# Kernel optimization log

Measured on AMD Instinct MI355X. Metric: run time of the kernel, lower is better.

Reference implementation:

```python
import jax, jax.numpy as jnp
import numpy as np
from jax import lax

N, H, W, C = 4, 256, 256, 128
COUT = 128
BS_IN, BS_OUT, BSTR = 18, 16, 16  # gather block, conv-out block, block stride
N_ACTIVE = 512


def setup_inputs() -> dict:
    key = jax.random.key(0)
    ks = jax.random.split(key, 8)
    x = jax.random.normal(ks[0], (N, H, W, C), dtype=jnp.float32)
    w = jax.random.normal(ks[1], (3, 3, C, COUT), dtype=jnp.float32) * 0.05  # HWIO
    b = jax.random.normal(ks[2], (COUT,), dtype=jnp.float32) * 0.05
    gamma = jax.random.uniform(ks[3], (COUT,), dtype=jnp.float32, minval=0.5, maxval=1.5)
    beta = jax.random.normal(ks[4], (COUT,), dtype=jnp.float32) * 0.1
    mean = jax.random.normal(ks[5], (COUT,), dtype=jnp.float32) * 0.1
    var = jax.random.uniform(ks[6], (COUT,), dtype=jnp.float32, minval=0.5, maxval=1.5)
    # unique active block ids over the N x (H/16) x (W/16) grid -> disjoint scatter targets
    n_blocks = N * (H // BSTR) * (W // BSTR)
    active = jax.random.permutation(ks[7], n_blocks)[:N_ACTIVE].astype(jnp.int32)
    return {"x": x, "w": w, "b": b, "gamma": gamma, "beta": beta,
            "mean": mean, "var": var, "active": active}


def reference(x, w, b, gamma, beta, mean, var, active):
    n_, h_, w_, c_ = x.shape
    nby, nbx = h_ // BSTR, w_ // BSTR
    bn = active // (nby * nbx)
    rem = active % (nby * nbx)
    by = rem // nbx
    bx = rem % nbx

    # --- sparse_gather: overlapping BS_IN x BS_IN input blocks (zero-pad edges) ---
    pad = BS_IN - BS_OUT
    xp = jnp.pad(x, ((0, 0), (0, pad), (0, pad), (0, 0)))
    Hp, Wp = h_ + pad, w_ + pad
    d_in = jnp.arange(BS_IN, dtype=jnp.int32)
    hs = by[:, None] * BSTR + d_in[None, :]            # [Nb, 18]
    ws = bx[:, None] * BSTR + d_in[None, :]            # [Nb, 18]
    gidx = bn[:, None, None] * (Hp * Wp) + hs[:, :, None] * Wp + ws[:, None, :]
    p = xp.reshape(-1, c_)[gidx]                       # [Nb, 18, 18, C]

    # --- dense conv + BN(eval, eps=1e-3) + ReLU on gathered blocks ---
    q = lax.conv_general_dilated(p, w, window_strides=(1, 1), padding='VALID',
                                 dimension_numbers=('NHWC', 'HWIO', 'NHWC'))
    q = q + b
    q = (q - mean) * (gamma * lax.rsqrt(var + 1e-3)) + beta
    q = jax.nn.relu(q)                                 # [Nb, 16, 16, COUT]

    # --- sparse_scatter: write disjoint BS_OUT blocks back into a copy of x ---
    d_out = jnp.arange(BS_OUT, dtype=jnp.int32)
    hso = by[:, None] * BSTR + d_out[None, :]
    wso = bx[:, None] * BSTR + d_out[None, :]
    sidx = bn[:, None, None] * (h_ * w_) + hso[:, :, None] * w_ + wso[:, None, :]
    y = x.reshape(-1, c_).at[sidx.reshape(-1)].set(q.reshape(-1, q.shape[-1]))
    return y.reshape(n_, h_, w_, c_)
```

## Files before the change

### kernel.cpp

```cpp
#include <hip/hip_runtime.h>
#include <hip/hip_bf16.h>

#define H_ 256
#define W_ 256
#define C_ 128
#define NBPOS 1024
#define NACT 512

typedef __bf16 bf16x8 __attribute__((ext_vector_type(8)));
typedef float f32x4 __attribute__((ext_vector_type(4)));

#define SCALE_OFF 294912
#define SHIFT_OFF 295424
#define FLAGS_OFF 295936

__global__ void prep_kernel(const float* __restrict__ w, const float* __restrict__ b,
                            const float* __restrict__ gamma, const float* __restrict__ beta,
                            const float* __restrict__ mean, const float* __restrict__ var,
                            const int* __restrict__ active,
                            __bf16* __restrict__ wprep, float* __restrict__ scale,
                            float* __restrict__ shift, int* __restrict__ flags) {
  int blk = blockIdx.x, tid = threadIdx.x;
  if (blk < 576) {
    int o = blk * 256 + tid;
    int j = o & 7, cout = (o >> 3) & 127, k8 = (o >> 10) & 15, tap = o >> 14;
    wprep[o] = (__bf16)w[((size_t)tap * 128 + k8 * 8 + j) * 128 + cout];
  } else {
    if (tid < 128) {
      float s = gamma[tid] * rsqrtf(var[tid] + 1e-3f);
      scale[tid] = s;
      shift[tid] = (b[tid] - mean[tid]) * s + beta[tid];
    }
    for (int i = tid; i < NACT; i += 256) flags[active[i]] = 1;
  }
}

__global__ __launch_bounds__(256, 2) void fused_kernel(
    const float* __restrict__ x, const __bf16* __restrict__ wprep,
    const float* __restrict__ scale, const float* __restrict__ shift,
    const int* __restrict__ flags, float* __restrict__ y) {
  __shared__ unsigned char ldsA[324 * 128];
  __shared__ unsigned char ldsB[2][8192];

  const int pb = blockIdx.x;
  const int tid = threadIdx.x;
  const int bn = pb >> 8, by = (pb >> 4) & 15, bx = pb & 15;
  const int h0 = by * 16, w0 = bx * 16;

  if (!flags[pb]) {
    size_t base4 = ((((size_t)bn * H_ + h0) * W_ + w0) * C_) >> 2;
    const float4* __restrict__ xs = (const float4*)x;
    float4* __restrict__ ys = (float4*)y;
#pragma unroll 8
    for (int i = 0; i < 32; ++i) {
      int lin = (i << 8) + tid;
      int row = lin >> 9, rem = lin & 511;
      size_t idx4 = base4 + (size_t)row * (W_ * C_ / 4) + rem;
      ys[idx4] = xs[idx4];
    }
    return;
  }

  const int lane = tid & 63;
  const int wid = tid >> 6;
  const float* xb = x + (size_t)bn * (H_ * W_ * C_);

  float sc[8], sh[8];
  {
    int col = lane & 15;
#pragma unroll
    for (int nb = 0; nb < 8; ++nb) {
      sc[nb] = scale[nb * 16 + col];
      sh[nb] = shift[nb * 16 + col];
    }
  }

  f32x4 acc[4][8];
  f32x4 zero = {0.f, 0.f, 0.f, 0.f};
#pragma unroll
  for (int i = 0; i < 4; ++i)
#pragma unroll
    for (int j = 0; j < 8; ++j) acc[i][j] = zero;

  const uint4* wp4 = (const uint4*)wprep;
  uint4 t0, t1;
  auto load_t = [&](int u) {
    int ks = u % 18, h = u / 18;
    int tile = ((ks >> 1) << 2) + (h << 1) + (ks & 1);
    t0 = wp4[tile * 512 + tid];
    t1 = wp4[tile * 512 + 256 + tid];
  };
  auto stage = [&](int half) {
    for (int chunk = tid; chunk < 324 * 8; chunk += 256) {
      int s = chunk >> 3, c8 = chunk & 7;
      int iy = s / 18, ix = s - iy * 18;
      int hs = h0 + iy, wsp = w0 + ix;
      float4 f0 = make_float4(0.f, 0.f, 0.f, 0.f), f1 = f0;
      if (hs < H_ && wsp < W_) {
        const float* p = xb + (size_t)(hs * W_ + wsp) * C_ + half * 64 + c8 * 8;
        f0 = *(const float4*)p;
        f1 = *(const float4*)(p + 4);
      }
      bf16x8 v;
      v[0] = (__bf16)f0.x; v[1] = (__bf16)f0.y; v[2] = (__bf16)f0.z; v[3] = (__bf16)f0.w;
      v[4] = (__bf16)f1.x; v[5] = (__bf16)f1.y; v[6] = (__bf16)f1.z; v[7] = (__bf16)f1.w;
      int lin = s * 128 + c8 * 16;
      *(bf16x8*)(&ldsA[lin ^ ((s & 7) << 4)]) = v;
    }
  };

  load_t(0);
  stage(0);
  ((uint4*)ldsB[0])[tid] = t0;
  ((uint4*)ldsB[0])[256 + tid] = t1;
  load_t(1);
  __syncthreads();

  const int koff = (lane >> 4) * 16;
  const int colb = (lane & 15) * 16;
  const int krow = (lane >> 4) * 2048;

  for (int u = 0; u < 36; ++u) {
    int cur = u & 1;
    if (u < 35) {
      ((uint4*)ldsB[cur ^ 1])[tid] = t0;
      ((uint4*)ldsB[cur ^ 1])[256 + tid] = t1;
      if (u < 34) load_t(u + 2);
    }
    int ks = u % 18;
    int tap = ks >> 1, kch = ks & 1;
    int dyv = tap / 3, dxv = tap - dyv * 3;

    bf16x8 a[4];
#pragma unroll
    for (int mi = 0; mi < 4; ++mi) {
      int srow = (wid * 4 + mi + dyv) * 18 + dxv + (lane & 15);
      int lin = srow * 128 + kch * 64 + koff;
      a[mi] = *(const bf16x8*)(&ldsA[lin ^ ((srow & 7) << 4)]);
    }
    bf16x8 bfr[8];
#pragma unroll
    for (int nb = 0; nb < 8; ++nb)
      bfr[nb] = *(const bf16x8*)(&ldsB[cur][krow + nb * 256 + colb]);
#pragma unroll
    for (int mi = 0; mi < 4; ++mi)
#pragma unroll
      for (int nb = 0; nb < 8; ++nb)
        acc[mi][nb] = __builtin_amdgcn_mfma_f32_16x16x32_bf16(a[mi], bfr[nb], acc[mi][nb], 0, 0, 0);

    __syncthreads();
    if (u == 17) {
      stage(1);
      __syncthreads();
    }
  }

  const int colc = lane & 15;
  float* yb = y + (((size_t)bn * H_ + h0) * W_ + w0) * C_;
#pragma unroll
  for (int mi = 0; mi < 4; ++mi) {
    int oy = wid * 4 + mi;
#pragma unroll
    for (int r = 0; r < 4; ++r) {
      int ox = (lane >> 4) * 4 + r;
      float* yr = yb + ((size_t)oy * W_ + ox) * C_;
#pragma unroll
      for (int nb = 0; nb < 8; ++nb) {
        float v = acc[mi][nb][r] * sc[nb] + sh[nb];
        yr[nb * 16 + colc] = fmaxf(v, 0.f);
      }
    }
  }
}

extern "C" void kernel_launch(void* const* d_in, const int* in_sizes, int n_in,
                              void* d_out, int out_size, void* d_ws, size_t ws_size,
                              hipStream_t stream) {
  const float* x     = (const float*)d_in[0];
  const float* w     = (const float*)d_in[1];
  const float* b     = (const float*)d_in[2];
  const float* gamma = (const float*)d_in[3];
  const float* beta  = (const float*)d_in[4];
  const float* mean  = (const float*)d_in[5];
  const float* var   = (const float*)d_in[6];
  const int*   act   = (const int*)d_in[7];
  float* y = (float*)d_out;
  char* ws = (char*)d_ws;
  __bf16* wprep = (__bf16*)ws;
  float* scale = (float*)(ws + SCALE_OFF);
  float* shift = (float*)(ws + SHIFT_OFF);
  int* flags = (int*)(ws + FLAGS_OFF);

  hipMemsetAsync(flags, 0, NBPOS * sizeof(int), stream);
  prep_kernel<<<dim3(577), dim3(256), 0, stream>>>(w, b, gamma, beta, mean, var, act,
                                                   wprep, scale, shift, flags);
  fused_kernel<<<dim3(NBPOS), dim3(256), 0, stream>>>(x, wprep, scale, shift, flags, y);
}
```

Before: 92.14 us.

## Split fused kernel into copy and compact conv kernels, load weights from global

Replaces the single fused kernel with two kernels. A copy kernel handles inactive blocks using nontemporal loads and stores. A conv kernel launches one workgroup per active block, indexed through the active list. The conv kernel drops the double-buffered LDS weight staging and reads weight fragments straight from global memory/L2, and it stages the input halves inside a simple loop. This removes divergent work within one grid and per-step LDS syncs, at the cost of an extra launch, losing overlap between copy and conv, and possibly higher global-load latency for the weights.

Result: no change. 93.68 us (+1.7%).

```diff
diff --git a/kernel.cpp b/kernel.cpp
--- a/kernel.cpp
+++ b/kernel.cpp
@@ -35,34 +35,39 @@
   }
 }
 
-__global__ __launch_bounds__(256, 2) void fused_kernel(
+__global__ __launch_bounds__(256) void copy_kernel(const float* __restrict__ x,
+                                                   const int* __restrict__ flags,
+                                                   float* __restrict__ y) {
+  int pb = blockIdx.x;
+  if (flags[pb]) return;
+  int bn = pb >> 8, by = (pb >> 4) & 15, bx = pb & 15;
+  size_t base4 = ((((size_t)bn * H_ + by * 16) * W_ + bx * 16) * C_) >> 2;
+  const f32x4* __restrict__ xs = (const f32x4*)x;
+  f32x4* __restrict__ ys = (f32x4*)y;
+#pragma unroll 4
+  for (int i = 0; i < 32; ++i) {
+    int lin = (i << 8) + threadIdx.x;
+    int row = lin >> 9, rem = lin & 511;
+    size_t idx4 = base4 + (size_t)row * (W_ * C_ / 4) + rem;
+    f32x4 v = __builtin_nontemporal_load(&xs[idx4]);
+    __builtin_nontemporal_store(v, &ys[idx4]);
+  }
+}
+
+__global__ __launch_bounds__(256, 2) void conv_kernel(
     const float* __restrict__ x, const __bf16* __restrict__ wprep,
     const float* __restrict__ scale, const float* __restrict__ shift,
-    const int* __restrict__ flags, float* __restrict__ y) {
+    const int* __restrict__ active, float* __restrict__ y) {
   __shared__ unsigned char ldsA[324 * 128];
-  __shared__ unsigned char ldsB[2][8192];
 
-  const int pb = blockIdx.x;
   const int tid = threadIdx.x;
-  const int bn = pb >> 8, by = (pb >> 4) & 15, bx = pb & 15;
-  const int h0 = by * 16, w0 = bx * 16;
-
-  if (!flags[pb]) {
-    size_t base4 = ((((size_t)bn * H_ + h0) * W_ + w0) * C_) >> 2;
-    const float4* __restrict__ xs = (const float4*)x;
-    float4* __restrict__ ys = (float4*)y;
-#pragma unroll 8
-    for (int i = 0; i < 32; ++i) {
-      int lin = (i << 8) + tid;
-      int row = lin >> 9, rem = lin & 511;
-      size_t idx4 = base4 + (size_t)row * (W_ * C_ / 4) + rem;
-      ys[idx4] = xs[idx4];
-    }
-    return;
-  }
-
   const int lane = tid & 63;
   const int wid = tid >> 6;
+  const int aid = active[blockIdx.x];
+  const int bn = aid >> 8;
+  const int by = (aid >> 4) & 15;
+  const int bx = aid & 15;
+  const int h0 = by * 16, w0 = bx * 16;
   const float* xb = x + (size_t)bn * (H_ * W_ * C_);
 
   float sc[8], sh[8];
@@ -82,15 +87,12 @@
 #pragma unroll
     for (int j = 0; j < 8; ++j) acc[i][j] = zero;
 
-  const uint4* wp4 = (const uint4*)wprep;
-  uint4 t0, t1;
-  auto load_t = [&](int u) {
-    int ks = u % 18, h = u / 18;
-    int tile = ((ks >> 1) << 2) + (h << 1) + (ks & 1);
-    t0 = wp4[tile * 512 + tid];
-    t1 = wp4[tile * 512 + 256 + tid];
-  };
-  auto stage = [&](int half) {
+  const bf16x8* __restrict__ wq = (const bf16x8*)wprep;
+  const int koff = (lane >> 4) * 16;
+  const int sbl = ((lane >> 4) << 7) + (lane & 15);
+
+  for (int half = 0; half < 2; ++half) {
+    __syncthreads();
     for (int chunk = tid; chunk < 324 * 8; chunk += 256) {
       int s = chunk >> 3, c8 = chunk & 7;
       int iy = s / 18, ix = s - iy * 18;
@@ -107,51 +109,31 @@
       int lin = s * 128 + c8 * 16;
       *(bf16x8*)(&ldsA[lin ^ ((s & 7) << 4)]) = v;
     }
-  };
+    __syncthreads();
 
-  load_t(0);
-  stage(0);
-  ((uint4*)ldsB[0])[tid] = t0;
-  ((uint4*)ldsB[0])[256 + tid] = t1;
-  load_t(1);
-  __syncthreads();
+#pragma unroll 2
+    for (int ks = 0; ks < 18; ++ks) {
+      int tap = ks >> 1, kch = ks & 1;
+      int dyv = tap / 3, dxv = tap - dyv * 3;
+      int tile = tap * 4 + half * 2 + kch;
 
-  const int koff = (lane >> 4) * 16;
-  const int colb = (lane & 15) * 16;
-  const int krow = (lane >> 4) * 2048;
-
-  for (int u = 0; u < 36; ++u) {
-    int cur = u & 1;
-    if (u < 35) {
-      ((uint4*)ldsB[cur ^ 1])[tid] = t0;
-      ((uint4*)ldsB[cur ^ 1])[256 + tid] = t1;
-      if (u < 34) load_t(u + 2);
-    }
-    int ks = u % 18;
-    int tap = ks >> 1, kch = ks & 1;
-    int dyv = tap / 3, dxv = tap - dyv * 3;
-
-    bf16x8 a[4];
+      bf16x8 a[4];
 #pragma unroll
-    for (int mi = 0; mi < 4; ++mi) {
-      int srow = (wid * 4 + mi + dyv) * 18 + dxv + (lane & 15);
-      int lin = srow * 128 + kch * 64 + koff;
-      a[mi] = *(const bf16x8*)(&ldsA[lin ^ ((srow & 7) << 4)]);
-    }
-    bf16x8 bfr[8];
-#pragma unroll
-    for (int nb = 0; nb < 8; ++nb)
-      bfr[nb] = *(const bf16x8*)(&ldsB[cur][krow + nb * 256 + colb]);
-#pragma unroll
-    for (int mi = 0; mi < 4; ++mi)
+      for (int mi = 0; mi < 4; ++mi) {
+        int srow = (wid * 4 + mi + dyv) * 18 + dxv + (lane & 15);
+        int lin = srow * 128 + kch * 64 + koff;
+        a[mi] = *(const bf16x8*)(&ldsA[lin ^ ((srow & 7) << 4)]);
+      }
+      bf16x8 bfr[8];
+      int sb = tile * 512 + sbl;
 #pragma unroll
       for (int nb = 0; nb < 8; ++nb)
-        acc[mi][nb] = __builtin_amdgcn_mfma_f32_16x16x32_bf16(a[mi], bfr[nb], acc[mi][nb], 0, 0, 0);
-
-    __syncthreads();
-    if (u == 17) {
-      stage(1);
-      __syncthreads();
+        bfr[nb] = wq[sb + nb * 16];
+#pragma unroll
+      for (int mi = 0; mi < 4; ++mi)
+#pragma unroll
+        for (int nb = 0; nb < 8; ++nb)
+          acc[mi][nb] = __builtin_amdgcn_mfma_f32_16x16x32_bf16(a[mi], bfr[nb], acc[mi][nb], 0, 0, 0);
     }
   }
 
@@ -167,7 +149,7 @@
 #pragma unroll
       for (int nb = 0; nb < 8; ++nb) {
         float v = acc[mi][nb][r] * sc[nb] + sh[nb];
-        yr[nb * 16 + colc] = fmaxf(v, 0.f);
+        __builtin_nontemporal_store(fmaxf(v, 0.f), &yr[nb * 16 + colc]);
       }
     }
   }
@@ -191,8 +173,9 @@
   float* shift = (float*)(ws + SHIFT_OFF);
   int* flags = (int*)(ws + FLAGS_OFF);
 
-  hipMemsetAsync(flags, 0, NBPOS * sizeof(int), stream);
+  (void)hipMemsetAsync(flags, 0, NBPOS * sizeof(int), stream);
   prep_kernel<<<dim3(577), dim3(256), 0, stream>>>(w, b, gamma, beta, mean, var, act,
                                                    wprep, scale, shift, flags);
-  fused_kernel<<<dim3(NBPOS), dim3(256), 0, stream>>>(x, wprep, scale, shift, flags, y);
+  copy_kernel<<<dim3(NBPOS), dim3(256), 0, stream>>>(x, flags, y);
+  conv_kernel<<<dim3(NACT), dim3(256), 0, stream>>>(x, wprep, scale, shift, act, y);
 }
```

## Pair each active conv block with an inactive copy block, interleaving copies

Applied to the files above, without the earlier changes.

Replaces the flag-based grid of 1024 blocks, where inactive blocks only copied x to y, with 512 blocks that each run one active conv and copy one inactive block. The copy is split into eight chunks whose loads and stores are spread across the MFMA loop, so memory traffic overlaps with compute. Copies and outputs use nontemporal loads and stores. The memset is replaced by a single-block kernel that builds the inactive list from a shared-memory bitmask. This relies on exactly 512 active and 512 inactive blocks, and it adds registers plus one extra launch.

Result: faster. 80.25 us (-12.9%).

```diff
diff --git a/kernel.cpp b/kernel.cpp
--- a/kernel.cpp
+++ b/kernel.cpp
@@ -12,58 +12,75 @@
 
 #define SCALE_OFF 294912
 #define SHIFT_OFF 295424
-#define FLAGS_OFF 295936
-
-__global__ void prep_kernel(const float* __restrict__ w, const float* __restrict__ b,
-                            const float* __restrict__ gamma, const float* __restrict__ beta,
-                            const float* __restrict__ mean, const float* __restrict__ var,
-                            const int* __restrict__ active,
-                            __bf16* __restrict__ wprep, float* __restrict__ scale,
-                            float* __restrict__ shift, int* __restrict__ flags) {
-  int blk = blockIdx.x, tid = threadIdx.x;
-  if (blk < 576) {
-    int o = blk * 256 + tid;
-    int j = o & 7, cout = (o >> 3) & 127, k8 = (o >> 10) & 15, tap = o >> 14;
-    wprep[o] = (__bf16)w[((size_t)tap * 128 + k8 * 8 + j) * 128 + cout];
-  } else {
-    if (tid < 128) {
-      float s = gamma[tid] * rsqrtf(var[tid] + 1e-3f);
-      scale[tid] = s;
-      shift[tid] = (b[tid] - mean[tid]) * s + beta[tid];
-    }
-    for (int i = tid; i < NACT; i += 256) flags[active[i]] = 1;
-  }
-}
-
-__global__ __launch_bounds__(256, 2) void fused_kernel(
+#define INACT_OFF 295936
+
+__global__ void prep_w_kernel(const float* __restrict__ w, __bf16* __restrict__ wprep) {
+  int o = blockIdx.x * 256 + threadIdx.x;
+  int j = o & 7, cout = (o >> 3) & 127, k8 = (o >> 10) & 15, tap = o >> 14;
+  wprep[o] = (__bf16)w[((size_t)tap * 128 + k8 * 8 + j) * 128 + cout];
+}
+
+__global__ void small_kernel(const float* __restrict__ b, const float* __restrict__ gamma,
+                             const float* __restrict__ beta, const float* __restrict__ mean,
+                             const float* __restrict__ var, const int* __restrict__ active,
+                             float* __restrict__ scale, float* __restrict__ shift,
+                             int* __restrict__ inact) {
+  __shared__ unsigned mask[32];
+  __shared__ int cnt;
+  int tid = threadIdx.x;
+  if (tid < 32) mask[tid] = 0u;
+  if (tid == 0) cnt = 0;
+  __syncthreads();
+  if (tid < NACT) {
+    int a = active[tid];
+    atomicOr(&mask[a >> 5], 1u << (a & 31));
+  }
+  if (tid < 128) {
+    float s = gamma[tid] * rsqrtf(var[tid] + 1e-3f);
+    scale[tid] = s;
+    shift[tid] = (b[tid] - mean[tid]) * s + beta[tid];
+  }
+  __syncthreads();
+  if (!((mask[tid >> 5] >> (tid & 31)) & 1u)) {
+    int p = atomicAdd(&cnt, 1);
+    inact[p] = tid;
+  }
+}
+
+__global__ __launch_bounds__(256, 2) void conv_kernel(
     const float* __restrict__ x, const __bf16* __restrict__ wprep,
     const float* __restrict__ scale, const float* __restrict__ shift,
-    const int* __restrict__ flags, float* __restrict__ y) {
+    const int* __restrict__ active, const int* __restrict__ inact,
+    float* __restrict__ y) {
   __shared__ unsigned char ldsA[324 * 128];
   __shared__ unsigned char ldsB[2][8192];
 
-  const int pb = blockIdx.x;
   const int tid = threadIdx.x;
-  const int bn = pb >> 8, by = (pb >> 4) & 15, bx = pb & 15;
-  const int h0 = by * 16, w0 = bx * 16;
-
-  if (!flags[pb]) {
-    size_t base4 = ((((size_t)bn * H_ + h0) * W_ + w0) * C_) >> 2;
-    const float4* __restrict__ xs = (const float4*)x;
-    float4* __restrict__ ys = (float4*)y;
-#pragma unroll 8
-    for (int i = 0; i < 32; ++i) {
-      int lin = (i << 8) + tid;
-      int row = lin >> 9, rem = lin & 511;
-      size_t idx4 = base4 + (size_t)row * (W_ * C_ / 4) + rem;
-      ys[idx4] = xs[idx4];
-    }
-    return;
-  }
-
   const int lane = tid & 63;
   const int wid = tid >> 6;
+  const int aid = active[blockIdx.x];
+  const int bn = aid >> 8, by = (aid >> 4) & 15, bx = aid & 15;
+  const int h0 = by * 16, w0 = bx * 16;
   const float* xb = x + (size_t)bn * (H_ * W_ * C_);
+
+  const int cid = inact[blockIdx.x];
+  const int cn = cid >> 8, cy = (cid >> 4) & 15, cx = cid & 15;
+  const size_t cbase4 = ((((size_t)cn * H_ + cy * 16) * W_ + cx * 16) * C_) >> 2;
+  const f32x4* __restrict__ xs = (const f32x4*)x;
+  f32x4* __restrict__ ys = (f32x4*)y;
+  f32x4 cbuf[4];
+  auto cidx = [&](int c, int k) -> size_t {
+    int lin = (c << 10) + (k << 8) + tid;
+    return cbase4 + (size_t)(lin >> 9) * (W_ * C_ / 4) + (lin & 511);
+  };
+  auto copy_load = [&](int c) {
+#pragma unroll
+    for (int k = 0; k < 4; ++k) cbuf[k] = __builtin_nontemporal_load(&xs[cidx(c, k)]);
+  };
+  auto copy_store = [&](int c) {
+#pragma unroll
+    for (int k = 0; k < 4; ++k) __builtin_nontemporal_store(cbuf[k], &ys[cidx(c, k)]);
+  };
 
   float sc[8], sh[8];
   {
@@ -110,6 +127,7 @@
   };
 
   load_t(0);
+  copy_load(0);
   stage(0);
   ((uint4*)ldsB[0])[tid] = t0;
   ((uint4*)ldsB[0])[256 + tid] = t1;
@@ -120,7 +138,13 @@
   const int colb = (lane & 15) * 16;
   const int krow = (lane >> 4) * 2048;
 
+  int cc = 0;
   for (int u = 0; u < 36; ++u) {
+    if (u == 5 || u == 10 || u == 15 || u == 19 || u == 24 || u == 28 || u == 33) {
+      copy_store(cc);
+      copy_load(cc + 1);
+      ++cc;
+    }
     int cur = u & 1;
     if (u < 35) {
       ((uint4*)ldsB[cur ^ 1])[tid] = t0;
@@ -154,6 +178,7 @@
       __syncthreads();
     }
   }
+  copy_store(7);
 
   const int colc = lane & 15;
   float* yb = y + (((size_t)bn * H_ + h0) * W_ + w0) * C_;
@@ -167,7 +192,7 @@
 #pragma unroll
       for (int nb = 0; nb < 8; ++nb) {
         float v = acc[mi][nb][r] * sc[nb] + sh[nb];
-        yr[nb * 16 + colc] = fmaxf(v, 0.f);
+        __builtin_nontemporal_store(fmaxf(v, 0.f), &yr[nb * 16 + colc]);
       }
     }
   }
@@ -189,10 +214,10 @@
   __bf16* wprep = (__bf16*)ws;
   float* scale = (float*)(ws + SCALE_OFF);
   float* shift = (float*)(ws + SHIFT_OFF);
-  int* flags = (int*)(ws + FLAGS_OFF);
-
-  hipMemsetAsync(flags, 0, NBPOS * sizeof(int), stream);
-  prep_kernel<<<dim3(577), dim3(256), 0, stream>>>(w, b, gamma, beta, mean, var, act,
-                                                   wprep, scale, shift, flags);
-  fused_kernel<<<dim3(NBPOS), dim3(256), 0, stream>>>(x, wprep, scale, shift, flags, y);
-}
+  int* inact = (int*)(ws + INACT_OFF);
+
+  prep_w_kernel<<<dim3(576), dim3(256), 0, stream>>>(w, wprep);
+  small_kernel<<<dim3(1), dim3(1024), 0, stream>>>(b, gamma, beta, mean, var, act,
+                                                   scale, shift, inact);
+  conv_kernel<<<dim3(NACT), dim3(256), 0, stream>>>(x, wprep, scale, shift, act, inact, y);
+}
```
